# Performance work log

Hardware: AMD Instinct MI355X
Metric: run time of the kernel (lower is better)

## Reference

```python
import jax, jax.numpy as jnp
import numpy as np

B, C, H, W = 64, 256, 32, 32


def setup_inputs() -> dict:
    key = jax.random.key(0)
    ks = jax.random.split(key, 7)
    x1 = jax.random.normal(ks[0], (B, C, H, W), dtype=jnp.float32)
    x2 = jax.random.normal(ks[1], (B, C, H, W), dtype=jnp.float32)
    # 1x1 Conv2d(C+1 -> C, bias=False): weight squeezed to (C, C+1)
    conv_w = jax.random.normal(ks[2], (C, C + 1), dtype=jnp.float32) * (1.0 / np.sqrt(C + 1))
    # caLayer: Conv1d(2->4, k=1) + ReLU + Conv1d(4->1, k=1) + Softmax(dim=1)
    ca_w1 = jax.random.normal(ks[3], (4, 2), dtype=jnp.float32) * (1.0 / np.sqrt(2))
    ca_b1 = jax.random.normal(ks[4], (4,), dtype=jnp.float32) * 0.1
    ca_w2 = jax.random.normal(ks[5], (1, 4), dtype=jnp.float32) * 0.5
    ca_b2 = jax.random.normal(ks[6], (1,), dtype=jnp.float32) * 0.1
    return {"x1": x1, "x2": x2, "conv_w": conv_w, "ca_w1": ca_w1,
            "ca_b1": ca_b1, "ca_w2": ca_w2, "ca_b2": ca_b2}


def _branch_pool(x, conv_w):
    # x: (B, C, H, W)
    b, c, h, w = x.shape
    center = x[:, :, h // 2, w // 2][:, :, None, None]          # (B, C, 1, 1)
    dot = jnp.sum(x * center, axis=1, keepdims=True) / c        # (B, 1, H, W)
    concatenated = jnp.concatenate([x, dot], axis=1)            # (B, C+1, H, W)
    attn = jax.nn.sigmoid(jnp.einsum('oc,bchw->bohw', conv_w, concatenated))
    norm = attn / (jnp.sum(attn, axis=(2, 3), keepdims=True) + 1e-8)
    return jnp.sum(x * norm, axis=(2, 3))                       # (B, C)


def reference(x1, x2, conv_w, ca_w1, ca_b1, ca_w2, ca_b2):
    pooled = jnp.stack([_branch_pool(x1, conv_w),
                        _branch_pool(x2, conv_w)], axis=1)      # (B, 2, C)
    # caLayer: kernel-size-1 Conv1d == channel-mixing matmul over axis 1
    h1 = jax.nn.relu(jnp.einsum('oi,bic->boc', ca_w1, pooled) + ca_b1[None, :, None])
    h2 = jnp.einsum('oi,bic->boc', ca_w2, h1) + ca_b2[None, :, None]  # (B, 1, C)
    x_weights = jax.nn.softmax(h2, axis=1)                      # softmax over size-1 dim
    y_total = pooled * x_weights                                # broadcast (B,2,C)
    return jnp.sum(y_total, axis=1)                             # (B, C)
```

## Files before the change

kernel.cpp:

```cpp
#include <hip/hip_runtime.h>
#include <hip/hip_bf16.h>
#include <math.h>

typedef __bf16 bf16x8 __attribute__((ext_vector_type(8)));
typedef float  f32x16 __attribute__((ext_vector_type(16)));

#define WLAST_OFF 32768
#define ACCA_OFF  65792
#define ACCX_OFF  98560

static __device__ __forceinline__ unsigned f2bf_u(float f) {
    unsigned u = __builtin_bit_cast(unsigned, f);
    return (u + 0x7fffu + ((u >> 16) & 1u)) >> 16;
}
static __device__ __forceinline__ unsigned pkbf(float a, float b) {
    __hip_bfloat162 h = __float22bfloat162_rn(make_float2(a, b));
    unsigned u; __builtin_memcpy(&u, &h, 4); return u;
}

static __device__ __forceinline__ void barrier_lds() {
    asm volatile("s_waitcnt lgkmcnt(0)\n\ts_barrier" ::: "memory");
}

template<int CTRL, int RM>
static __device__ __forceinline__ float dpp_add(float x) {
    int yi = __builtin_amdgcn_update_dpp(0, __builtin_bit_cast(int, x), CTRL, RM, 0xF, true);
    return x + __builtin_bit_cast(float, yi);
}
static __device__ __forceinline__ float red32(float x) {
    x = dpp_add<0x121, 0xF>(x);
    x = dpp_add<0x122, 0xF>(x);
    x = dpp_add<0x124, 0xF>(x);
    x = dpp_add<0x128, 0xF>(x);
    x = dpp_add<0x142, 0xA>(x);
    return x;
}

__global__ void k_init(const float* __restrict__ conv_w, float* __restrict__ ws) {
    int bk = blockIdx.x;
    int tid = threadIdx.x;
    int idx = bk * 256 + tid;
    int j  = idx & 7;
    int l  = (idx >> 3) & 63;
    int ot = (idx >> 9) & 7;
    int S  = idx >> 12;
    int o  = ot * 32 + (l & 31);
    int k  = S * 16 + (l >> 5) * 8 + j;
    ((unsigned short*)ws)[idx] = (unsigned short)f2bf_u(conv_w[o * 257 + k]);
    if (idx < 256) ws[WLAST_OFF + idx] = conv_w[idx * 257 + 256];
    ws[ACCA_OFF + idx] = 0.0f;
}

__global__ __launch_bounds__(512, 2)
void k_main(const float* __restrict__ x1, const float* __restrict__ x2,
            float* __restrict__ ws) {
    int bx = blockIdx.x;
    int xb = bx >> 1;
    int half = bx & 1;
    const float* xpi = ((xb < 64) ? x1 : x2) + (size_t)(xb & 63) * (256 * 1024);
    const unsigned short* wfrag = (const unsigned short*)ws;
    float* accA = ws + ACCA_OFF + xb * 256;
    float* accX = ws + ACCX_OFF + xb * 256;

    int tid = threadIdx.x;
    int w = tid >> 6;
    int l = tid & 63;
    int lw = l & 31, q = l >> 5;

    __shared__ __align__(16) unsigned sx[16][64][8];
    __shared__ float sd[64][9];
    __shared__ float swl[256];
    __shared__ float scen[256];
    __shared__ float dotf[64];

    int hwi = tid & 15, kc = tid >> 4;

    float cenv = 0.f, wlv = 0.f;
    if (tid < 256) {
        cenv = xpi[(size_t)tid * 1024 + 528];
        wlv  = ws[WLAST_OFF + tid];
    }
    const unsigned short* ap = wfrag + (size_t)(w * 64 + l) * 8;
    bf16x8 A[16];
    #pragma unroll
    for (int S = 0; S < 16; ++S)
        A[S] = *(const bf16x8*)(ap + (size_t)S * 4096);

    const float* xbase = xpi + half * 512 + (size_t)(kc * 2) * 1024 + hwi * 4;
    float4 xv[8];
    #pragma unroll
    for (int s = 0; s < 4; ++s) {
        xv[2 * s]     = *(const float4*)(xbase + (size_t)(64 * s) * 1024);
        xv[2 * s + 1] = *(const float4*)(xbase + (size_t)(64 * s + 1) * 1024);
    }
    if (tid < 256) { scen[tid] = cenv; swl[tid] = wlv; }
    barrier_lds();

    int sig = ((lw >> 4) & 1) << 2;
    const unsigned* b0p = &sx[0][lw][(q * 4) ^ sig];
    const unsigned* b1p = &sx[0][32 + lw][(q * 4) ^ sig];

    float sA[16], sX[16];
    #pragma unroll
    for (int r = 0; r < 16; ++r) { sA[r] = 0.f; sX[r] = 0.f; }

    #pragma unroll 1
    for (int t = 0; t < 8; ++t) {
        if (t) barrier_lds();

        float dotp[4] = {0.f, 0.f, 0.f, 0.f};
        #pragma unroll
        for (int s = 0; s < 4; ++s) {
            float4 e = xv[2 * s], o4 = xv[2 * s + 1];
            int c = kc * 2 + 64 * s;
            float s0 = scen[c], s1 = scen[c + 1];
            dotp[0] += e.x * s0 + o4.x * s1;
            dotp[1] += e.y * s0 + o4.y * s1;
            dotp[2] += e.z * s0 + o4.z * s1;
            dotp[3] += e.w * s0 + o4.w * s1;
            int S  = (kc >> 3) + 4 * s;
            int wd = kc & 7;
            float ee[4] = {e.x, e.y, e.z, e.w};
            float oo[4] = {o4.x, o4.y, o4.z, o4.w};
            #pragma unroll
            for (int j = 0; j < 4; ++j) {
                int jj  = (hwi + j) & 3;
                int hwr = hwi * 4 + jj;
                sx[S][hwr][wd ^ (((hwr >> 4) & 1) << 2)] = pkbf(ee[jj], oo[jj]);
            }
        }
        if (t < 7) {
            const float* xn = xbase + (t + 1) * 64;
            #pragma unroll
            for (int s = 0; s < 4; ++s) {
                xv[2 * s]     = *(const float4*)(xn + (size_t)(64 * s) * 1024);
                xv[2 * s + 1] = *(const float4*)(xn + (size_t)(64 * s + 1) * 1024);
            }
        }
        #pragma unroll
        for (int j = 0; j < 4; ++j) {
            float v = dotp[j];
            v += __shfl_xor(v, 16, 64);
            v += __shfl_xor(v, 32, 64);
            dotp[j] = v;
        }
        if (l < 16) {
            #pragma unroll
            for (int j = 0; j < 4; ++j) sd[hwi * 4 + j][w] = dotp[j];
        }
        barrier_lds();

        if (tid < 64) {
            float ssum = 0.f;
            #pragma unroll
            for (int k2 = 0; k2 < 8; ++k2) ssum += sd[tid][k2];
            dotf[tid] = ssum * (1.0f / 256.0f);
        }

        f32x16 acc0, acc1;
        #pragma unroll
        for (int e = 0; e < 16; ++e) { acc0[e] = 0.0f; acc1[e] = 0.0f; }
        #pragma unroll
        for (int S = 0; S < 16; ++S) {
            bf16x8 b0, b1;
            __builtin_memcpy(&b0, b0p + S * 512, 16);
            __builtin_memcpy(&b1, b1p + S * 512, 16);
            acc0 = __builtin_amdgcn_mfma_f32_32x32x16_bf16(A[S], b0, acc0, 0, 0, 0);
            acc1 = __builtin_amdgcn_mfma_f32_32x32x16_bf16(A[S], b1, acc1, 0, 0, 0);
        }
        barrier_lds();

        float dv0 = dotf[lw];
        float dv1 = dotf[32 + lw];
        #pragma unroll
        for (int r = 0; r < 16; ++r) {
            int row = (r & 3) + 8 * (r >> 2) + 4 * q;
            int o = w * 32 + row;
            float wl = swl[o];
            float z0 = acc0[r] + wl * dv0;
            float z1 = acc1[r] + wl * dv1;
            float a0s = __builtin_amdgcn_rcpf(1.0f + __expf(-z0));
            float a1s = __builtin_amdgcn_rcpf(1.0f + __expf(-z1));
            int Si = o >> 4, wd = (o >> 1) & 7;
            unsigned w0 = sx[Si][lw][wd ^ sig];
            unsigned w1 = sx[Si][32 + lw][wd ^ sig];
            float xv0, xv1;
            if (o & 1) {
                xv0 = __builtin_bit_cast(float, w0 & 0xffff0000u);
                xv1 = __builtin_bit_cast(float, w1 & 0xffff0000u);
            } else {
                xv0 = __builtin_bit_cast(float, w0 << 16);
                xv1 = __builtin_bit_cast(float, w1 << 16);
            }
            sA[r] += a0s + a1s;
            sX[r] += a0s * xv0 + a1s * xv1;
        }
    }

    #pragma unroll
    for (int r = 0; r < 16; ++r) {
        int row = (r & 3) + 8 * (r >> 2) + 4 * q;
        int o = w * 32 + row;
        float rA = red32(sA[r]);
        float rX = red32(sX[r]);
        if (lw == 31) {
            atomicAdd(&accA[o], rA);
            atomicAdd(&accX[o], rX);
        }
    }
}

__global__ void k_out(const float* __restrict__ ws, float* __restrict__ out) {
    int idx = blockIdx.x * 256 + threadIdx.x;
    int b = idx >> 8, o = idx & 255;
    float a0 = ws[ACCA_OFF + b * 256 + o];
    float p0 = ws[ACCX_OFF + b * 256 + o];
    float a1 = ws[ACCA_OFF + (64 + b) * 256 + o];
    float p1 = ws[ACCX_OFF + (64 + b) * 256 + o];
    out[idx] = p0 / (a0 + 1e-8f) + p1 / (a1 + 1e-8f);
}

extern "C" void kernel_launch(void* const* d_in, const int* in_sizes, int n_in,
                              void* d_out, int out_size, void* d_ws, size_t ws_size,
                              hipStream_t stream) {
    const float* x1     = (const float*)d_in[0];
    const float* x2     = (const float*)d_in[1];
    const float* conv_w = (const float*)d_in[2];
    float* ws  = (float*)d_ws;
    float* out = (float*)d_out;

    k_init<<<256, 256, 0, stream>>>(conv_w, ws);
    k_main<<<256, 512, 0, stream>>>(x1, x2, ws);
    k_out<<<64, 256, 0, stream>>>(ws, out);
}
```

Baseline: 163.9 us.

## Double-buffer LDS tiles to overlap next-tile conversion with MFMA compute

Splits the shared bf16 staging buffer and the dot buffer into two halves so the conversion of tile t+1 (packing to bf16, partial dot with the center vector) happens right after the MFMAs of tile t, and the global prefetch moves two tiles ahead. This cuts one barrier per iteration and lets LDS writes and ALU work overlap the matrix-core work. The epilogue also reads the x values as 8-byte pairs instead of separate 4-byte reads. The cost is double the LDS footprint (about 64KB for sx), which may limit occupancy at 2 blocks per CU, plus more register pressure.

New measurement: 164.6 us. No clear change (+0.4%).

```diff
diff --git a/kernel.cpp b/kernel.cpp
--- a/kernel.cpp
+++ b/kernel.cpp
@@ -67,11 +67,11 @@
     int l = tid & 63;
     int lw = l & 31, q = l >> 5;
 
-    __shared__ __align__(16) unsigned sx[16][64][8];
+    __shared__ __align__(16) unsigned sx[2][16][64][8];
     __shared__ float sd[64][9];
     __shared__ float swl[256];
     __shared__ float scen[256];
-    __shared__ float dotf[64];
+    __shared__ float dotf[2][64];
 
     int hwi = tid & 15, kc = tid >> 4;
 
@@ -97,17 +97,8 @@
     barrier_lds();
 
     int sig = ((lw >> 4) & 1) << 2;
-    const unsigned* b0p = &sx[0][lw][(q * 4) ^ sig];
-    const unsigned* b1p = &sx[0][32 + lw][(q * 4) ^ sig];
-
-    float sA[16], sX[16];
-    #pragma unroll
-    for (int r = 0; r < 16; ++r) { sA[r] = 0.f; sX[r] = 0.f; }
-
-    #pragma unroll 1
-    for (int t = 0; t < 8; ++t) {
-        if (t) barrier_lds();
-
+
+    auto do_convert = [&](int buf) {
         float dotp[4] = {0.f, 0.f, 0.f, 0.f};
         #pragma unroll
         for (int s = 0; s < 4; ++s) {
@@ -126,15 +117,7 @@
             for (int j = 0; j < 4; ++j) {
                 int jj  = (hwi + j) & 3;
                 int hwr = hwi * 4 + jj;
-                sx[S][hwr][wd ^ (((hwr >> 4) & 1) << 2)] = pkbf(ee[jj], oo[jj]);
-            }
-        }
-        if (t < 7) {
-            const float* xn = xbase + (t + 1) * 64;
-            #pragma unroll
-            for (int s = 0; s < 4; ++s) {
-                xv[2 * s]     = *(const float4*)(xn + (size_t)(64 * s) * 1024);
-                xv[2 * s + 1] = *(const float4*)(xn + (size_t)(64 * s + 1) * 1024);
+                sx[buf][S][hwr][wd ^ (((hwr >> 4) & 1) << 2)] = pkbf(ee[jj], oo[jj]);
             }
         }
         #pragma unroll
@@ -148,18 +131,40 @@
             #pragma unroll
             for (int j = 0; j < 4; ++j) sd[hwi * 4 + j][w] = dotp[j];
         }
-        barrier_lds();
-
-        if (tid < 64) {
-            float ssum = 0.f;
-            #pragma unroll
-            for (int k2 = 0; k2 < 8; ++k2) ssum += sd[tid][k2];
-            dotf[tid] = ssum * (1.0f / 256.0f);
-        }
+    };
+    auto do_prefetch = [&](int ct) {
+        const float* xn = xbase + ct * 64;
+        #pragma unroll
+        for (int s = 0; s < 4; ++s) {
+            xv[2 * s]     = *(const float4*)(xn + (size_t)(64 * s) * 1024);
+            xv[2 * s + 1] = *(const float4*)(xn + (size_t)(64 * s + 1) * 1024);
+        }
+    };
+
+    do_convert(0);
+    do_prefetch(1);
+    barrier_lds();
+    if (tid < 64) {
+        float ssum = 0.f;
+        #pragma unroll
+        for (int k2 = 0; k2 < 8; ++k2) ssum += sd[tid][k2];
+        dotf[0][tid] = ssum * (1.0f / 256.0f);
+    }
+    barrier_lds();
+
+    float sA[16], sX[16];
+    #pragma unroll
+    for (int r = 0; r < 16; ++r) { sA[r] = 0.f; sX[r] = 0.f; }
+
+    #pragma unroll 1
+    for (int t = 0; t < 8; ++t) {
+        int cur = t & 1, nxt = cur ^ 1;
 
         f32x16 acc0, acc1;
         #pragma unroll
         for (int e = 0; e < 16; ++e) { acc0[e] = 0.0f; acc1[e] = 0.0f; }
+        const unsigned* b0p = &sx[cur][0][lw][(q * 4) ^ sig];
+        const unsigned* b1p = &sx[cur][0][32 + lw][(q * 4) ^ sig];
         #pragma unroll
         for (int S = 0; S < 16; ++S) {
             bf16x8 b0, b1;
@@ -168,33 +173,46 @@
             acc0 = __builtin_amdgcn_mfma_f32_32x32x16_bf16(A[S], b0, acc0, 0, 0, 0);
             acc1 = __builtin_amdgcn_mfma_f32_32x32x16_bf16(A[S], b1, acc1, 0, 0, 0);
         }
+        if (t < 7) do_convert(nxt);
+        if (t < 6) do_prefetch(t + 2);
         barrier_lds();
 
-        float dv0 = dotf[lw];
-        float dv1 = dotf[32 + lw];
-        #pragma unroll
-        for (int r = 0; r < 16; ++r) {
-            int row = (r & 3) + 8 * (r >> 2) + 4 * q;
-            int o = w * 32 + row;
-            float wl = swl[o];
-            float z0 = acc0[r] + wl * dv0;
-            float z1 = acc1[r] + wl * dv1;
-            float a0s = __builtin_amdgcn_rcpf(1.0f + __expf(-z0));
-            float a1s = __builtin_amdgcn_rcpf(1.0f + __expf(-z1));
-            int Si = o >> 4, wd = (o >> 1) & 7;
-            unsigned w0 = sx[Si][lw][wd ^ sig];
-            unsigned w1 = sx[Si][32 + lw][wd ^ sig];
-            float xv0, xv1;
-            if (o & 1) {
-                xv0 = __builtin_bit_cast(float, w0 & 0xffff0000u);
-                xv1 = __builtin_bit_cast(float, w1 & 0xffff0000u);
-            } else {
-                xv0 = __builtin_bit_cast(float, w0 << 16);
-                xv1 = __builtin_bit_cast(float, w1 << 16);
+        if (t < 7 && tid < 64) {
+            float ssum = 0.f;
+            #pragma unroll
+            for (int k2 = 0; k2 < 8; ++k2) ssum += sd[tid][k2];
+            dotf[nxt][tid] = ssum * (1.0f / 256.0f);
+        }
+        float dv0 = dotf[cur][lw];
+        float dv1 = dotf[cur][32 + lw];
+        #pragma unroll
+        for (int m = 0; m < 4; ++m) {
+            int ob = w * 32 + 8 * m + 4 * q;
+            int Si = ob >> 4;
+            int Wp = ((ob >> 1) & 7) ^ sig;
+            unsigned u0[2], u1[2];
+            __builtin_memcpy(u0, &sx[cur][Si][lw][Wp], 8);
+            __builtin_memcpy(u1, &sx[cur][Si][32 + lw][Wp], 8);
+            #pragma unroll
+            for (int d = 0; d < 4; ++d) {
+                int r = 4 * m + d;
+                int o = ob + d;
+                float wl = swl[o];
+                float z0 = acc0[r] + wl * dv0;
+                float z1 = acc1[r] + wl * dv1;
+                float a0s = __builtin_amdgcn_rcpf(1.0f + __expf(-z0));
+                float a1s = __builtin_amdgcn_rcpf(1.0f + __expf(-z1));
+                unsigned wa = (d & 2) ? u0[1] : u0[0];
+                unsigned wb = (d & 2) ? u1[1] : u1[0];
+                float xv0 = (d & 1) ? __builtin_bit_cast(float, wa & 0xffff0000u)
+                                    : __builtin_bit_cast(float, wa << 16);
+                float xv1 = (d & 1) ? __builtin_bit_cast(float, wb & 0xffff0000u)
+                                    : __builtin_bit_cast(float, wb << 16);
+                sA[r] += a0s + a1s;
+                sX[r] += a0s * xv0 + a1s * xv1;
             }
-            sA[r] += a0s + a1s;
-            sX[r] += a0s * xv0 + a1s * xv1;
-        }
+        }
+        barrier_lds();
     }
 
     #pragma unroll
```

## Split each image into quarters across more blocks and vectorize LDS x reads

Applied to the files above, without the earlier changes.

The grid goes from 256 to 512 blocks, each covering a quarter of the spatial positions (4 tiles instead of 8), and launch bounds request 4 blocks per CU. This should fill all CUs on the device and raise occupancy, at the cost of reloading the weight fragments and center values twice as many times and doubling the atomic traffic. The epilogue also reads bf16 x values from LDS with one 8-byte load per group of four rows instead of four 4-byte loads. The tighter launch bound may force register spills given the 16 bf16x8 A fragments held per thread.

After: 224.5 us. +37.0%, slower.

```diff
diff --git a/kernel.cpp b/kernel.cpp
--- a/kernel.cpp
+++ b/kernel.cpp
@@ -51,12 +51,12 @@
     ws[ACCA_OFF + idx] = 0.0f;
 }
 
-__global__ __launch_bounds__(512, 2)
+__global__ __launch_bounds__(512, 4)
 void k_main(const float* __restrict__ x1, const float* __restrict__ x2,
             float* __restrict__ ws) {
     int bx = blockIdx.x;
-    int xb = bx >> 1;
-    int half = bx & 1;
+    int xb = bx >> 2;
+    int qr = bx & 3;
     const float* xpi = ((xb < 64) ? x1 : x2) + (size_t)(xb & 63) * (256 * 1024);
     const unsigned short* wfrag = (const unsigned short*)ws;
     float* accA = ws + ACCA_OFF + xb * 256;
@@ -86,7 +86,7 @@
     for (int S = 0; S < 16; ++S)
         A[S] = *(const bf16x8*)(ap + (size_t)S * 4096);
 
-    const float* xbase = xpi + half * 512 + (size_t)(kc * 2) * 1024 + hwi * 4;
+    const float* xbase = xpi + qr * 256 + (size_t)(kc * 2) * 1024 + hwi * 4;
     float4 xv[8];
     #pragma unroll
     for (int s = 0; s < 4; ++s) {
@@ -105,7 +105,7 @@
     for (int r = 0; r < 16; ++r) { sA[r] = 0.f; sX[r] = 0.f; }
 
     #pragma unroll 1
-    for (int t = 0; t < 8; ++t) {
+    for (int t = 0; t < 4; ++t) {
         if (t) barrier_lds();
 
         float dotp[4] = {0.f, 0.f, 0.f, 0.f};
@@ -129,7 +129,7 @@
                 sx[S][hwr][wd ^ (((hwr >> 4) & 1) << 2)] = pkbf(ee[jj], oo[jj]);
             }
         }
-        if (t < 7) {
+        if (t < 3) {
             const float* xn = xbase + (t + 1) * 64;
             #pragma unroll
             for (int s = 0; s < 4; ++s) {
@@ -173,27 +173,31 @@
         float dv0 = dotf[lw];
         float dv1 = dotf[32 + lw];
         #pragma unroll
-        for (int r = 0; r < 16; ++r) {
-            int row = (r & 3) + 8 * (r >> 2) + 4 * q;
-            int o = w * 32 + row;
-            float wl = swl[o];
-            float z0 = acc0[r] + wl * dv0;
-            float z1 = acc1[r] + wl * dv1;
-            float a0s = __builtin_amdgcn_rcpf(1.0f + __expf(-z0));
-            float a1s = __builtin_amdgcn_rcpf(1.0f + __expf(-z1));
-            int Si = o >> 4, wd = (o >> 1) & 7;
-            unsigned w0 = sx[Si][lw][wd ^ sig];
-            unsigned w1 = sx[Si][32 + lw][wd ^ sig];
-            float xv0, xv1;
-            if (o & 1) {
-                xv0 = __builtin_bit_cast(float, w0 & 0xffff0000u);
-                xv1 = __builtin_bit_cast(float, w1 & 0xffff0000u);
-            } else {
-                xv0 = __builtin_bit_cast(float, w0 << 16);
-                xv1 = __builtin_bit_cast(float, w1 << 16);
+        for (int m = 0; m < 4; ++m) {
+            int ob = w * 32 + 8 * m + 4 * q;
+            int Si = ob >> 4;
+            int Wp = ((ob >> 1) & 7) ^ sig;
+            unsigned u0[2], u1[2];
+            __builtin_memcpy(u0, &sx[Si][lw][Wp], 8);
+            __builtin_memcpy(u1, &sx[Si][32 + lw][Wp], 8);
+            #pragma unroll
+            for (int d = 0; d < 4; ++d) {
+                int r = 4 * m + d;
+                int o = ob + d;
+                float wl = swl[o];
+                float z0 = acc0[r] + wl * dv0;
+                float z1 = acc1[r] + wl * dv1;
+                float a0s = __builtin_amdgcn_rcpf(1.0f + __expf(-z0));
+                float a1s = __builtin_amdgcn_rcpf(1.0f + __expf(-z1));
+                unsigned wa = (d & 2) ? u0[1] : u0[0];
+                unsigned wb = (d & 2) ? u1[1] : u1[0];
+                float xv0 = (d & 1) ? __builtin_bit_cast(float, wa & 0xffff0000u)
+                                    : __builtin_bit_cast(float, wa << 16);
+                float xv1 = (d & 1) ? __builtin_bit_cast(float, wb & 0xffff0000u)
+                                    : __builtin_bit_cast(float, wb << 16);
+                sA[r] += a0s + a1s;
+                sX[r] += a0s * xv0 + a1s * xv1;
             }
-            sA[r] += a0s + a1s;
-            sX[r] += a0s * xv0 + a1s * xv1;
         }
     }
 
@@ -230,6 +234,6 @@
     float* out = (float*)d_out;
 
     k_init<<<256, 256, 0, stream>>>(conv_w, ws);
-    k_main<<<256, 512, 0, stream>>>(x1, x2, ws);
+    k_main<<<512, 512, 0, stream>>>(x1, x2, ws);
     k_out<<<64, 256, 0, stream>>>(ws, out);
 }
```
